# Performance work log

Hardware: AMD Instinct MI355X
Metric: run time of the kernel (lower is better)

The kernel has to match this reference:

```python
import jax, jax.numpy as jnp
import numpy as np

MAX_VAL = 1e4  # kornia geodesic border pad value for erosion


def _erode(img, k):
    # img: [B, Cs, H, W]; flat all-ones structuring element => sliding-window min
    pad_lo = k // 2
    pad_hi = k - pad_lo - 1
    padded = jnp.pad(
        img,
        ((0, 0), (0, 0), (pad_lo, pad_hi), (pad_lo, pad_hi)),
        constant_values=MAX_VAL,
    )
    return jax.lax.reduce_window(
        padded,
        jnp.inf,
        jax.lax.min,
        window_dimensions=(1, 1, k, k),
        window_strides=(1, 1, 1, 1),
        padding='VALID',
    )


def setup_inputs() -> dict:
    key = jax.random.key(0)
    B, C, H, W = 8, 64, 512, 512
    x = jax.random.normal(key, (B, C, H, W), dtype=jnp.float32)
    indices = jnp.arange(32, dtype=jnp.int32)  # channel subset to erode
    return {"x": x, "indices": indices, "k": 3}


def reference(x, indices, k):
    sub = x[:, indices]            # [B, 32, H, W] gather of selected channels
    eroded = _erode(sub, k)        # windowed min (erosion with ones kernel)
    return x.at[:, indices].set(eroded)
```

## Files before the change

### kernel.cpp

```cpp
#include <hip/hip_runtime.h>

#define MAX_VAL 10000.0f

__global__ __launch_bounds__(256) void erode_kernel(
    const float* __restrict__ x,
    const int* __restrict__ indices, int n_idx,
    float* __restrict__ out)
{
    unsigned idx = blockIdx.x * 256u + threadIdx.x;
    unsigned w4 = idx & 127u;
    unsigned h  = (idx >> 7) & 511u;
    unsigned bc = idx >> 16;
    unsigned c  = bc & 63u;

    __shared__ int s_flag;
    if (threadIdx.x == 0) {
        int f = 0;
        for (int i = 0; i < n_idx; ++i) f |= (indices[i] == (int)c);
        s_flag = f;
    }
    __syncthreads();

    const float* plane  = x   + (size_t)bc * (512u * 512u);
    float*       oplane = out + (size_t)bc * (512u * 512u);
    unsigned w0 = w4 * 4u;
    const float* src = plane + (size_t)h * 512u + w0;
    float* dst = oplane + (size_t)h * 512u + w0;

    if (!s_flag) {
        *(float4*)dst = *(const float4*)src;
        return;
    }

    float4 vm = make_float4(MAX_VAL, MAX_VAL, MAX_VAL, MAX_VAL);
    float lm = MAX_VAL, rm = MAX_VAL;
    const bool has_l = (w0 > 0);
    const bool has_r = (w0 + 4u < 512u);

#pragma unroll
    for (int dh = -1; dh <= 1; ++dh) {
        int hh = (int)h + dh;
        if (hh < 0 || hh >= 512) continue;
        const float* row = plane + (size_t)hh * 512u;
        float4 v = *(const float4*)(row + w0);
        vm.x = fminf(vm.x, v.x);
        vm.y = fminf(vm.y, v.y);
        vm.z = fminf(vm.z, v.z);
        vm.w = fminf(vm.w, v.w);
        if (has_l) lm = fminf(lm, row[w0 - 1]);
        if (has_r) rm = fminf(rm, row[w0 + 4]);
    }

    float4 r;
    r.x = fminf(fminf(lm,   vm.x), vm.y);
    r.y = fminf(fminf(vm.x, vm.y), vm.z);
    r.z = fminf(fminf(vm.y, vm.z), vm.w);
    r.w = fminf(fminf(vm.z, vm.w), rm);
    *(float4*)dst = r;
}

extern "C" void kernel_launch(void* const* d_in, const int* in_sizes, int n_in,
                              void* d_out, int out_size, void* d_ws, size_t ws_size,
                              hipStream_t stream) {
    const float* x       = (const float*)d_in[0];
    const int*   indices = (const int*)d_in[1];
    int n_idx = in_sizes[1];
    float* out = (float*)d_out;

    unsigned n_groups = 8u * 64u * 512u * 512u / 4u;
    dim3 grid(n_groups / 256u), block(256);
    erode_kernel<<<grid, block, 0, stream>>>(x, indices, n_idx, out);
}
```

Measured before the change: 890.3 us.

## Process 8-row strips per thread with rolling separable min and parallel flag scan

```diff
diff --git a/kernel.cpp b/kernel.cpp
--- a/kernel.cpp
+++ b/kernel.cpp
@@ -7,56 +7,67 @@
     const int* __restrict__ indices, int n_idx,
     float* __restrict__ out)
 {
-    unsigned idx = blockIdx.x * 256u + threadIdx.x;
-    unsigned w4 = idx & 127u;
-    unsigned h  = (idx >> 7) & 511u;
-    unsigned bc = idx >> 16;
-    unsigned c  = bc & 63u;
+    const unsigned tid   = threadIdx.x;
+    const unsigned w4    = tid & 127u;
+    const unsigned S     = blockIdx.x * 2u + (tid >> 7);
+    const unsigned bc    = S >> 6;
+    const unsigned strip = S & 63u;
+    const unsigned h0    = strip * 8u;
+    const unsigned c     = bc & 63u;
+    const unsigned w0    = w4 * 4u;
 
     __shared__ int s_flag;
-    if (threadIdx.x == 0) {
-        int f = 0;
-        for (int i = 0; i < n_idx; ++i) f |= (indices[i] == (int)c);
-        s_flag = f;
-    }
+    if (tid == 0) s_flag = 0;
+    __syncthreads();
+    for (unsigned i = tid; i < (unsigned)n_idx; i += 256u)
+        if (indices[i] == (int)c) s_flag = 1;
     __syncthreads();
 
     const float* plane  = x   + (size_t)bc * (512u * 512u);
     float*       oplane = out + (size_t)bc * (512u * 512u);
-    unsigned w0 = w4 * 4u;
-    const float* src = plane + (size_t)h * 512u + w0;
-    float* dst = oplane + (size_t)h * 512u + w0;
+    const float* ip = plane  + (size_t)h0 * 512u + w0;
+    float*       op = oplane + (size_t)h0 * 512u + w0;
 
     if (!s_flag) {
-        *(float4*)dst = *(const float4*)src;
+#pragma unroll
+        for (int r = 0; r < 8; ++r)
+            *(float4*)(op + r * 512) = *(const float4*)(ip + r * 512);
         return;
     }
 
-    float4 vm = make_float4(MAX_VAL, MAX_VAL, MAX_VAL, MAX_VAL);
-    float lm = MAX_VAL, rm = MAX_VAL;
     const bool has_l = (w0 > 0);
     const bool has_r = (w0 + 4u < 512u);
 
-#pragma unroll
-    for (int dh = -1; dh <= 1; ++dh) {
-        int hh = (int)h + dh;
-        if (hh < 0 || hh >= 512) continue;
+    auto hrow = [&](int hh) -> float4 {
+        float4 h;
+        if (hh < 0 || hh > 511) {
+            h.x = h.y = h.z = h.w = MAX_VAL;
+            return h;
+        }
         const float* row = plane + (size_t)hh * 512u;
         float4 v = *(const float4*)(row + w0);
-        vm.x = fminf(vm.x, v.x);
-        vm.y = fminf(vm.y, v.y);
-        vm.z = fminf(vm.z, v.z);
-        vm.w = fminf(vm.w, v.w);
-        if (has_l) lm = fminf(lm, row[w0 - 1]);
-        if (has_r) rm = fminf(rm, row[w0 + 4]);
+        float ll = has_l ? row[w0 - 1] : MAX_VAL;
+        float rr = has_r ? row[w0 + 4] : MAX_VAL;
+        h.x = fminf(ll,  fminf(v.x, v.y));
+        h.y = fminf(v.x, fminf(v.y, v.z));
+        h.z = fminf(v.y, fminf(v.z, v.w));
+        h.w = fminf(v.z, fminf(v.w, rr));
+        return h;
+    };
+
+    float4 a = hrow((int)h0 - 1);
+    float4 b = hrow((int)h0);
+#pragma unroll
+    for (int r = 0; r < 8; ++r) {
+        float4 d = hrow((int)h0 + r + 1);
+        float4 o;
+        o.x = fminf(a.x, fminf(b.x, d.x));
+        o.y = fminf(a.y, fminf(b.y, d.y));
+        o.z = fminf(a.z, fminf(b.z, d.z));
+        o.w = fminf(a.w, fminf(b.w, d.w));
+        *(float4*)(op + r * 512) = o;
+        a = b; b = d;
     }
-
-    float4 r;
-    r.x = fminf(fminf(lm,   vm.x), vm.y);
-    r.y = fminf(fminf(vm.x, vm.y), vm.z);
-    r.z = fminf(fminf(vm.y, vm.z), vm.w);
-    r.w = fminf(fminf(vm.z, vm.w), rm);
-    *(float4*)dst = r;
 }
 
 extern "C" void kernel_launch(void* const* d_in, const int* in_sizes, int n_in,
@@ -67,7 +78,6 @@
     int n_idx = in_sizes[1];
     float* out = (float*)d_out;
 
-    unsigned n_groups = 8u * 64u * 512u * 512u / 4u;
-    dim3 grid(n_groups / 256u), block(256);
+    dim3 grid(16384), block(256);
     erode_kernel<<<grid, block, 0, stream>>>(x, indices, n_idx, out);
 }
```

Result: faster. 842.4 us (-5.4%).
